# Performance work log

Hardware: AMD Instinct MI355X
Metric: run time of the kernel (lower is better)

## Reference

```python
import jax, jax.numpy as jnp
import numpy as np

N = 100_000
E = 1_600_000
D_IN, D_HID, D_OUT = 512, 256, 256


def setup_inputs() -> dict:
    key = jax.random.key(0)
    ks = jax.random.split(key, 10)
    x = jax.random.normal(ks[0], (N, D_IN), dtype=jnp.float32)
    edge_index = jax.random.randint(ks[1], (2, E), 0, N, dtype=jnp.int64)
    edge_weight = jax.random.uniform(ks[2], (E,), dtype=jnp.float32)
    # Glorot-ish init for the per-layer linear weights (PyG GCNConv: Linear w/o bias, bias added after aggregation)
    W1 = jax.random.normal(ks[3], (D_IN, D_HID), dtype=jnp.float32) * (1.0 / np.sqrt(D_IN))
    b1 = jnp.zeros((D_HID,), dtype=jnp.float32)
    W2 = jax.random.normal(ks[4], (D_HID, D_HID), dtype=jnp.float32) * (1.0 / np.sqrt(D_HID))
    b2 = jnp.zeros((D_HID,), dtype=jnp.float32)
    W3 = jax.random.normal(ks[5], (D_HID, D_OUT), dtype=jnp.float32) * (1.0 / np.sqrt(D_HID))
    b3 = jnp.zeros((D_OUT,), dtype=jnp.float32)
    return {"x": x, "edge_index": edge_index, "edge_weight": edge_weight,
            "W1": W1, "b1": b1, "W2": W2, "b2": b2, "W3": W3, "b3": b3}


def gcn_layer(h_in, W, b, row, col, ew, n):
    # PyG GCNConv with normalize=True, add_self_loops=True (fill value 1.0), aggr='add':
    # h = X W; deg[i] = sum of incoming edge weights (incl. self loop);
    # norm_e = deg^-1/2[row] * w_e * deg^-1/2[col]; out[col] += norm_e * h[row]; out += bias
    h = h_in @ W                                            # [n, d_out]
    deg = jnp.zeros((n,), h.dtype).at[col].add(ew) + 1.0    # +1 from self loop
    dinv = jnp.where(deg > 0, jax.lax.rsqrt(deg), 0.0)      # deg_inv_sqrt, inf -> 0
    norm = dinv[row] * ew * dinv[col]                       # [E]
    out = jnp.zeros_like(h).at[col].add(norm[:, None] * h[row])
    out = out + (dinv * dinv)[:, None] * h                  # self-loop contribution (norm_ii = dinv_i^2)
    return out + b


def reference(x, edge_index, edge_weight, W1, b1, W2, b2, W3, b3):
    row, col = edge_index[0], edge_index[1]
    n = x.shape[0]
    # dropout p=0.0 -> identity
    h = jax.nn.relu(gcn_layer(x, W1, b1, row, col, edge_weight, n))
    h = jax.nn.relu(gcn_layer(h, W2, b2, row, col, edge_weight, n))
    return gcn_layer(h, W3, b3, row, col, edge_weight, n)
```

## Files before the change

### kernel.cpp

```cpp
#include <hip/hip_runtime.h>
#include <hip/hip_bf16.h>


#define D 256
#define ELLW 48
#define BSH2 9
#define NB2MAX 256
#define DEPTH 24
#define GCAP 8960
#define FIXSCALE 1099511627776.0f
#define FIXINV   9.094947017729282e-13

typedef unsigned short ushort_t;
typedef unsigned long long u64;
typedef float f32x2 __attribute__((ext_vector_type(2)));
typedef float f32x4 __attribute__((ext_vector_type(4)));
typedef short bf16x8 __attribute__((ext_vector_type(8)));
typedef unsigned int u32x4 __attribute__((ext_vector_type(4)));

__device__ __forceinline__ float blo(unsigned u) { return __uint_as_float(u << 16); }
__device__ __forceinline__ float bhi(unsigned u) { return __uint_as_float(u & 0xFFFF0000u); }
__device__ __forceinline__ ushort_t f2b(float f) {
    unsigned u = __float_as_uint(f);
    return (ushort_t)((u + 0x7FFFu + ((u >> 16) & 1u)) >> 16);
}
__device__ __forceinline__ void gload_lds16(const ushort_t* g, ushort_t* l) {
    __builtin_amdgcn_global_load_lds((const __attribute__((address_space(1))) unsigned int*)g,
                                     (__attribute__((address_space(3))) unsigned int*)l, 16, 0, 0);
}

__global__ void zero_gfill(int* __restrict__ gfill, int nb) {
    if ((int)threadIdx.x < nb) gfill[threadIdx.x] = 0;
}

__global__ __launch_bounds__(1024) void bin_p1(const int* __restrict__ row,
                                               const int* __restrict__ col,
                                               const float* __restrict__ ew,
                                               int* __restrict__ gfill,
                                               u64* __restrict__ bins, int E, int nb) {
    __shared__ u64 lbuf[196][DEPTH];
    __shared__ int lcnt[196];
    __shared__ int sgp[196];
    const int t = threadIdx.x;
    const int wv = t >> 6, ln = t & 63;
    if (t < 196) lcnt[t] = 0;
    __syncthreads();
    int per = (E + gridDim.x - 1) / gridDim.x;
    int e0 = blockIdx.x * per;
    int e1 = e0 + per;
    if (e1 > E) e1 = E;
    for (int base = e0; base < e1; base += 1024) {
        int e = base + t;
        if (e < e1) {
            int c = __builtin_nontemporal_load(&col[e]);
            int r = __builtin_nontemporal_load(&row[e]);
            float w = __builtin_nontemporal_load(&ew[e]);
            int b = c >> BSH2;
            u64 rec = ((u64)__float_as_uint(w) << 32) | ((u64)(unsigned)r << 9) |
                      (unsigned)(c & ((1 << BSH2) - 1));
            int pos = atomicAdd(&lcnt[b], 1);
            if (pos < DEPTH) {
                lbuf[b][pos] = rec;
            } else {
                int gp = atomicAdd(&gfill[b], 1);
                if (gp < GCAP) bins[(size_t)b * GCAP + gp] = rec;
                atomicSub(&lcnt[b], 1);
            }
        }
        __syncthreads();
        if (t < nb) {
            int c = lcnt[t];
            int k8 = c & ~7;
            sgp[t] = (k8 > 0) ? atomicAdd(&gfill[t], k8) : 0;
        }
        __syncthreads();
        for (int b = wv; b < nb; b += 16) {
            int c = lcnt[b];
            int k8 = c & ~7;
            if (k8 > 0) {
                int gp = sgp[b];
                if (ln < k8) {
                    int idx = gp + ln;
                    if (idx < GCAP) bins[(size_t)b * GCAP + idx] = lbuf[b][ln];
                }
                int rem = c - k8;
                u64 mv = (ln < rem) ? lbuf[b][k8 + ln] : 0ull;
                if (ln < rem) lbuf[b][ln] = mv;
                if (ln == 0) lcnt[b] = rem;
            }
        }
        __syncthreads();
    }
    if (t < nb) {
        int c = lcnt[t];
        sgp[t] = (c > 0) ? atomicAdd(&gfill[t], c) : 0;
    }
    __syncthreads();
    for (int b = wv; b < nb; b += 16) {
        int c = lcnt[b];
        if (c > 0) {
            int gp = sgp[b];
            if (ln < c) {
                int idx = gp + ln;
                if (idx < GCAP) bins[(size_t)b * GCAP + idx] = lbuf[b][ln];
            }
        }
    }
}

__global__ __launch_bounds__(512) void bin_p2(const u64* __restrict__ bins,
                                              const int* __restrict__ gfill,
                                              int* __restrict__ cnt,
                                              float* __restrict__ dinv,
                                              u64* __restrict__ ell, int N) {
    __shared__ u64 sacc[1 << BSH2];
    const int b = blockIdx.x, t = threadIdx.x;
    const int base = b << BSH2;
    for (int i = t; i < (1 << BSH2); i += 512) sacc[i] = 0ull;
    __syncthreads();
    int fill = gfill[b];
    if (fill > GCAP) fill = GCAP;
    for (int i = t; i < fill; i += 512) {
        u64 rec = bins[(size_t)b * GCAP + i];
        int li = (int)(rec & ((1 << BSH2) - 1));
        unsigned r = (unsigned)((rec >> 9) & 0x1FFFFu);
        unsigned wb = (unsigned)(rec >> 32);
        u64 pack = (1ull << 48) | (u64)(__uint_as_float(wb) * FIXSCALE);
        int pos = (int)(atomicAdd(&sacc[li], pack) >> 48);
        if (pos < ELLW)
            ell[(size_t)(base + li) * ELLW + pos] = ((u64)wb << 32) | r;
    }
    __syncthreads();
    for (int i = t; i < (1 << BSH2); i += 512) {
        int node = base + i;
        if (node < N) {
            u64 p = sacc[i];
            int m = (int)(p >> 48);
            cnt[node] = (m > ELLW) ? ELLW : m;
            float sum = (float)((double)(p & 0xFFFFFFFFFFFFull) * FIXINV);
            dinv[node] = rsqrtf(sum + 1.0f);
        }
    }
}

__global__ __launch_bounds__(256) void cvtT_kernel(const float* __restrict__ W,
                                                   ushort_t* __restrict__ WT, int K, int C) {
    int i = blockIdx.x * 256 + threadIdx.x;
    if (i < K * C) {
        int c = i / K, k = i - c * K;
        WT[i] = f2b(W[(size_t)k * C + c]);
    }
}

template <int K, bool AF32>
__global__ __launch_bounds__(256) void gemm_mfma(const void* __restrict__ Ap,
                                                 const ushort_t* __restrict__ WT,
                                                 ushort_t* __restrict__ C, int nvalid) {
    __shared__ ushort_t As[128 * 64];
    __shared__ ushort_t Bs[256 * 64];
    const int tid = threadIdx.x;
    const int lane = tid & 63, wave = tid >> 6;
    const int wrow = wave >> 1, wcol = wave & 1;
    const int fr = lane & 15, fq = lane >> 4;
    const int r0 = blockIdx.x * 128;

    f32x4 acc[4][8] = {};

    for (int k0 = 0; k0 < K; k0 += 64) {
        if constexpr (AF32) {
            const float* Af = (const float*)Ap;
#pragma unroll
            for (int i = 0; i < 8; ++i) {
                int idx = i * 256 + tid;
                int rowt = idx >> 4;
                int c4 = idx & 15;
                int grow = r0 + rowt;
                if (grow >= nvalid) grow = nvalid - 1;
                f32x4 v = __builtin_nontemporal_load(
                    (const f32x4*)&Af[(size_t)grow * K + k0 + c4 * 4]);
                __hip_bfloat162 b01 = __float22bfloat162_rn(make_float2(v[0], v[1]));
                __hip_bfloat162 b23 = __float22bfloat162_rn(make_float2(v[2], v[3]));
                uint2 st = make_uint2(*(unsigned*)&b01, *(unsigned*)&b23);
                int slot = c4 >> 1, half = c4 & 1;
                int off = rowt * 64 + ((slot ^ (rowt & 7)) << 3) + (half << 2);
                *(uint2*)&As[off] = st;
            }
        } else {
            const ushort_t* Ab = (const ushort_t*)Ap;
#pragma unroll
            for (int q = 0; q < 4; ++q) {
                int qa = wave * 4 + q;
                int rowt = qa * 8 + (lane >> 3);
                int g = (lane & 7) ^ (lane >> 3);
                gload_lds16(&Ab[(size_t)(r0 + rowt) * K + k0 + g * 8], &As[qa * 512]);
            }
        }
#pragma unroll
        for (int q = 0; q < 8; ++q) {
            int qb = wave * 8 + q;
            int rowt = qb * 8 + (lane >> 3);
            int g = (lane & 7) ^ (lane >> 3);
            gload_lds16(&WT[(size_t)rowt * K + k0 + g * 8], &Bs[qb * 512]);
        }
        __syncthreads();

#pragma unroll
        for (int kk = 0; kk < 2; ++kk) {
            int g = (kk * 4 + fq) ^ (fr & 7);
            bf16x8 aF[4];
#pragma unroll
            for (int m = 0; m < 4; ++m) {
                int arow = wrow * 64 + m * 16 + fr;
                aF[m] = *(const bf16x8*)&As[arow * 64 + g * 8];
            }
#pragma unroll
            for (int n = 0; n < 8; ++n) {
                int bcol = wcol * 128 + n * 16 + fr;
                bf16x8 bF = *(const bf16x8*)&Bs[bcol * 64 + g * 8];
#pragma unroll
                for (int m = 0; m < 4; ++m)
                    acc[m][n] = __builtin_amdgcn_mfma_f32_16x16x32_bf16(
                        bF, aF[m], acc[m][n], 0, 0, 0);
            }
        }
        __syncthreads();
    }

#pragma unroll
    for (int m = 0; m < 4; ++m) {
        int gr = r0 + wrow * 64 + m * 16 + fr;
        if (gr < nvalid) {
#pragma unroll
            for (int n = 0; n < 8; ++n) {
                ushort4 h;
                h.x = f2b(acc[m][n][0]); h.y = f2b(acc[m][n][1]);
                h.z = f2b(acc[m][n][2]); h.w = f2b(acc[m][n][3]);
                *(ushort4*)&C[(size_t)gr * D + wcol * 128 + n * 16 + fq * 4] = h;
            }
        }
    }
}

template <bool NORM, bool RELU, bool OUTF32>
__global__ __launch_bounds__(256) void agg_kernel(const ushort_t* __restrict__ hb,
                                                  const float* __restrict__ dinv,
                                                  const float* __restrict__ bias,
                                                  const int* __restrict__ cnt,
                                                  u64* __restrict__ ell,
                                                  void* __restrict__ outp, int N) {
    int node = blockIdx.x * 4 + (threadIdx.x >> 6);
    if (node >= N) return;
    int lane = threadIdx.x & 63;
    int half = lane >> 5;
    int fl = lane & 31;
    float dn = dinv[node], d2 = dn * dn;

    u32x4 sv = *(const u32x4*)&hb[(size_t)node * 256 + fl * 8];
    float sc = half ? 0.f : d2;
    float a0 = sc * blo(sv.x), a1 = sc * bhi(sv.x);
    float a2 = sc * blo(sv.y), a3 = sc * bhi(sv.y);
    float a4 = sc * blo(sv.z), a5 = sc * bhi(sv.z);
    float a6 = sc * blo(sv.w), a7 = sc * bhi(sv.w);

    int m = cnt[node];
    int srcl = 0;
    float wl = 0.f;
    if (lane < m) {
        u64 r = ell[(size_t)node * ELLW + lane];
        srcl = (int)(unsigned)r;
        float w = __uint_as_float((unsigned)(r >> 32));
        if (NORM) {
            wl = dinv[srcl] * w * dn;
            ell[(size_t)node * ELLW + lane] =
                ((u64)__float_as_uint(wl) << 32) | (unsigned)srcl;
        } else {
            wl = w;
        }
    }
    int steps = (m + 1) >> 1;
#pragma unroll 8
    for (int j = 0; j < steps; ++j) {
        int idx2 = 2 * j + half;
        int src = __shfl(srcl, idx2);
        float w = __shfl(wl, idx2);
        u32x4 v = *(const u32x4*)&hb[(size_t)src * 256 + fl * 8];
        a0 = fmaf(w, blo(v.x), a0); a1 = fmaf(w, bhi(v.x), a1);
        a2 = fmaf(w, blo(v.y), a2); a3 = fmaf(w, bhi(v.y), a3);
        a4 = fmaf(w, blo(v.z), a4); a5 = fmaf(w, bhi(v.z), a5);
        a6 = fmaf(w, blo(v.w), a6); a7 = fmaf(w, bhi(v.w), a7);
    }
    a0 += __shfl_xor(a0, 32); a1 += __shfl_xor(a1, 32);
    a2 += __shfl_xor(a2, 32); a3 += __shfl_xor(a3, 32);
    a4 += __shfl_xor(a4, 32); a5 += __shfl_xor(a5, 32);
    a6 += __shfl_xor(a6, 32); a7 += __shfl_xor(a7, 32);
    float r0 = half ? a4 : a0;
    float r1 = half ? a5 : a1;
    float r2 = half ? a6 : a2;
    float r3 = half ? a7 : a3;
    f32x4 bb = *(const f32x4*)&bias[fl * 8 + half * 4];
    r0 += bb[0]; r1 += bb[1]; r2 += bb[2]; r3 += bb[3];
    if (RELU) {
        r0 = fmaxf(r0, 0.f); r1 = fmaxf(r1, 0.f);
        r2 = fmaxf(r2, 0.f); r3 = fmaxf(r3, 0.f);
    }
    if (OUTF32) {
        f32x4 o = {r0, r1, r2, r3};
        __builtin_nontemporal_store(
            o, (f32x4*)((float*)outp + (size_t)node * 256 + fl * 8 + half * 4));
    } else {
        u64 p = (u64)f2b(r0) | ((u64)f2b(r1) << 16) | ((u64)f2b(r2) << 32) | ((u64)f2b(r3) << 48);
        __builtin_nontemporal_store(
            p, (u64*)((ushort_t*)outp + (size_t)node * 256 + fl * 8 + half * 4));
    }
}

extern "C" void kernel_launch(void* const* d_in, const int* in_sizes, int n_in,
                              void* d_out, int out_size, void* d_ws, size_t ws_size,
                              hipStream_t stream) {
    const float* x  = (const float*)d_in[0];
    const int*   ei = (const int*)d_in[1];
    const float* ew = (const float*)d_in[2];
    const float* W1 = (const float*)d_in[3];
    const float* b1 = (const float*)d_in[4];
    const float* W2 = (const float*)d_in[5];
    const float* b2 = (const float*)d_in[6];
    const float* W3 = (const float*)d_in[7];
    const float* b3 = (const float*)d_in[8];
    const int N = in_sizes[0] / 512;
    const int E = in_sizes[2];
    const int* row = ei;
    const int* col = ei + E;
    float* out = (float*)d_out;

    const int MB = (N + 127) / 128;
    const size_t Npad = (size_t)MB * 128;
    const int NB2 = (N + (1 << BSH2) - 1) >> BSH2;

    char* ws = (char*)d_ws;
    size_t off = 0;
    auto alloc = [&](size_t bytes) -> void* {
        void* p = ws + off;
        off += (bytes + 255) / 256 * 256;
        return p;
    };
    ushort_t* hb  = (ushort_t*)alloc(Npad * D * sizeof(ushort_t));
    u64*      ell = (u64*)alloc((size_t)N * ELLW * sizeof(u64));
    ushort_t* WT1 = (ushort_t*)alloc((size_t)512 * D * sizeof(ushort_t));
    ushort_t* WT2 = (ushort_t*)alloc((size_t)256 * D * sizeof(ushort_t));
    ushort_t* WT3 = (ushort_t*)alloc((size_t)256 * D * sizeof(ushort_t));
    int*   cnt    = (int*)alloc((size_t)N * sizeof(int));
    float* dinv   = (float*)alloc((size_t)N * sizeof(float));
    int*   gfill  = (int*)alloc((size_t)NB2MAX * sizeof(int));
    u64*   bins   = (u64*)hb;
    ushort_t* ab  = (ushort_t*)d_out;

    int gA = (N + 3) / 4;
    zero_gfill<<<1, 256, 0, stream>>>(gfill, NB2);
    cvtT_kernel<<<(512 * D + 255) / 256, 256, 0, stream>>>(W1, WT1, 512, D);
    cvtT_kernel<<<(256 * D + 255) / 256, 256, 0, stream>>>(W2, WT2, 256, D);
    cvtT_kernel<<<(256 * D + 255) / 256, 256, 0, stream>>>(W3, WT3, 256, D);
    bin_p1<<<256, 1024, 0, stream>>>(row, col, ew, gfill, bins, E, NB2);
    bin_p2<<<NB2, 512, 0, stream>>>(bins, gfill, cnt, dinv, ell, N);

    gemm_mfma<512, true><<<MB, 256, 0, stream>>>(x, WT1, hb, N);
    agg_kernel<true, true, false><<<gA, 256, 0, stream>>>(hb, dinv, b1, cnt, ell, ab, N);
    gemm_mfma<256, false><<<MB, 256, 0, stream>>>(ab, WT2, hb, N);
    agg_kernel<false, true, false><<<gA, 256, 0, stream>>>(hb, dinv, b2, cnt, ell, ab, N);
    gemm_mfma<256, false><<<MB, 256, 0, stream>>>(ab, WT3, hb, N);
    agg_kernel<false, false, true><<<gA, 256, 0, stream>>>(hb, dinv, b3, cnt, ell, out, N);
}
```

Before: 635.4 us.

## Co-schedule edge binning with first GEMM in one heterogeneous kernel launch

Merges the three weight transpose/convert kernels and the gfill zeroing into a single prep kernel. Edge binning (now 512 blocks of 256 threads with a smaller local buffer depth) and the first-layer GEMM then run in one launch, with block IDs split between the two roles so the memory-bound binning overlaps the compute-bound GEMM. Because hb can no longer double as the bins buffer, bins get their own workspace allocation. The cost is extra workspace, plus possible imbalance or lower occupancy from the shared 48KB LDS footprint in the binning blocks.

```diff
diff --git a/kernel.cpp b/kernel.cpp
--- a/kernel.cpp
+++ b/kernel.cpp
@@ -6,7 +6,8 @@
 #define ELLW 48
 #define BSH2 9
 #define NB2MAX 256
-#define DEPTH 24
+#define DEPTH 16
+#define NBIN 512
 #define GCAP 8960
 #define FIXSCALE 1099511627776.0f
 #define FIXINV   9.094947017729282e-13
@@ -29,27 +30,47 @@
                                      (__attribute__((address_space(3))) unsigned int*)l, 16, 0, 0);
 }
 
-__global__ void zero_gfill(int* __restrict__ gfill, int nb) {
-    if ((int)threadIdx.x < nb) gfill[threadIdx.x] = 0;
-}
-
-__global__ __launch_bounds__(1024) void bin_p1(const int* __restrict__ row,
-                                               const int* __restrict__ col,
-                                               const float* __restrict__ ew,
-                                               int* __restrict__ gfill,
-                                               u64* __restrict__ bins, int E, int nb) {
-    __shared__ u64 lbuf[196][DEPTH];
-    __shared__ int lcnt[196];
-    __shared__ int sgp[196];
+__global__ __launch_bounds__(256) void prep_kernel(const float* __restrict__ W1,
+                                                   const float* __restrict__ W2,
+                                                   const float* __restrict__ W3,
+                                                   ushort_t* __restrict__ WT1,
+                                                   ushort_t* __restrict__ WT2,
+                                                   ushort_t* __restrict__ WT3,
+                                                   int* __restrict__ gfill, int nb) {
+    int i = blockIdx.x * 256 + threadIdx.x;
+    if (i < nb) gfill[i] = 0;
+    if (i < 131072) {
+        int c = i >> 9, k = i & 511;
+        WT1[i] = f2b(W1[k * 256 + c]);
+    } else if (i < 196608) {
+        int j = i - 131072;
+        int c = j >> 8, k = j & 255;
+        WT2[j] = f2b(W2[k * 256 + c]);
+    } else if (i < 262144) {
+        int j = i - 196608;
+        int c = j >> 8, k = j & 255;
+        WT3[j] = f2b(W3[k * 256 + c]);
+    }
+}
+
+__device__ __forceinline__ void bin_body(char* smem,
+                                         const int* __restrict__ row,
+                                         const int* __restrict__ col,
+                                         const float* __restrict__ ew,
+                                         int* __restrict__ gfill,
+                                         u64* __restrict__ bins, int E, int nb, int bid) {
+    u64 (*lbuf)[DEPTH] = (u64(*)[DEPTH])smem;
+    int* lcnt = (int*)(smem + 25088);
+    int* sgp  = (int*)(smem + 25088 + 784);
     const int t = threadIdx.x;
     const int wv = t >> 6, ln = t & 63;
     if (t < 196) lcnt[t] = 0;
     __syncthreads();
-    int per = (E + gridDim.x - 1) / gridDim.x;
-    int e0 = blockIdx.x * per;
+    int per = (E + NBIN - 1) / NBIN;
+    int e0 = bid * per;
     int e1 = e0 + per;
     if (e1 > E) e1 = E;
-    for (int base = e0; base < e1; base += 1024) {
+    for (int base = e0; base < e1; base += 256) {
         int e = base + t;
         if (e < e1) {
             int c = __builtin_nontemporal_load(&col[e]);
@@ -74,7 +95,7 @@
             sgp[t] = (k8 > 0) ? atomicAdd(&gfill[t], k8) : 0;
         }
         __syncthreads();
-        for (int b = wv; b < nb; b += 16) {
+        for (int b = wv; b < nb; b += 4) {
             int c = lcnt[b];
             int k8 = c & ~7;
             if (k8 > 0) {
@@ -96,7 +117,7 @@
         sgp[t] = (c > 0) ? atomicAdd(&gfill[t], c) : 0;
     }
     __syncthreads();
-    for (int b = wv; b < nb; b += 16) {
+    for (int b = wv; b < nb; b += 4) {
         int c = lcnt[b];
         if (c > 0) {
             int gp = sgp[b];
@@ -106,6 +127,121 @@
             }
         }
     }
+}
+
+template <int K, bool AF32>
+__device__ __forceinline__ void gemm_body(char* smem,
+                                          const void* __restrict__ Ap,
+                                          const ushort_t* __restrict__ WT,
+                                          ushort_t* __restrict__ C, int nvalid, int tile) {
+    ushort_t* As = (ushort_t*)smem;
+    ushort_t* Bs = (ushort_t*)(smem + 16384);
+    const int tid = threadIdx.x;
+    const int lane = tid & 63, wave = tid >> 6;
+    const int wrow = wave >> 1, wcol = wave & 1;
+    const int fr = lane & 15, fq = lane >> 4;
+    const int r0 = tile * 128;
+
+    f32x4 acc[4][8] = {};
+
+    for (int k0 = 0; k0 < K; k0 += 64) {
+        if constexpr (AF32) {
+            const float* Af = (const float*)Ap;
+#pragma unroll
+            for (int i = 0; i < 8; ++i) {
+                int idx = i * 256 + tid;
+                int rowt = idx >> 4;
+                int c4 = idx & 15;
+                int grow = r0 + rowt;
+                if (grow >= nvalid) grow = nvalid - 1;
+                f32x4 v = __builtin_nontemporal_load(
+                    (const f32x4*)&Af[(size_t)grow * K + k0 + c4 * 4]);
+                __hip_bfloat162 b01 = __float22bfloat162_rn(make_float2(v[0], v[1]));
+                __hip_bfloat162 b23 = __float22bfloat162_rn(make_float2(v[2], v[3]));
+                uint2 st = make_uint2(*(unsigned*)&b01, *(unsigned*)&b23);
+                int slot = c4 >> 1, half = c4 & 1;
+                int off = rowt * 64 + ((slot ^ (rowt & 7)) << 3) + (half << 2);
+                *(uint2*)&As[off] = st;
+            }
+        } else {
+            const ushort_t* Ab = (const ushort_t*)Ap;
+#pragma unroll
+            for (int q = 0; q < 4; ++q) {
+                int qa = wave * 4 + q;
+                int rowt = qa * 8 + (lane >> 3);
+                int g = (lane & 7) ^ (lane >> 3);
+                gload_lds16(&Ab[(size_t)(r0 + rowt) * K + k0 + g * 8], &As[qa * 512]);
+            }
+        }
+#pragma unroll
+        for (int q = 0; q < 8; ++q) {
+            int qb = wave * 8 + q;
+            int rowt = qb * 8 + (lane >> 3);
+            int g = (lane & 7) ^ (lane >> 3);
+            gload_lds16(&WT[(size_t)rowt * K + k0 + g * 8], &Bs[qb * 512]);
+        }
+        __syncthreads();
+
+#pragma unroll
+        for (int kk = 0; kk < 2; ++kk) {
+            int g = (kk * 4 + fq) ^ (fr & 7);
+            bf16x8 aF[4];
+#pragma unroll
+            for (int m = 0; m < 4; ++m) {
+                int arow = wrow * 64 + m * 16 + fr;
+                aF[m] = *(const bf16x8*)&As[arow * 64 + g * 8];
+            }
+#pragma unroll
+            for (int n = 0; n < 8; ++n) {
+                int bcol = wcol * 128 + n * 16 + fr;
+                bf16x8 bF = *(const bf16x8*)&Bs[bcol * 64 + g * 8];
+#pragma unroll
+                for (int m = 0; m < 4; ++m)
+                    acc[m][n] = __builtin_amdgcn_mfma_f32_16x16x32_bf16(
+                        bF, aF[m], acc[m][n], 0, 0, 0);
+            }
+        }
+        __syncthreads();
+    }
+
+#pragma unroll
+    for (int m = 0; m < 4; ++m) {
+        int gr = r0 + wrow * 64 + m * 16 + fr;
+        if (gr < nvalid) {
+#pragma unroll
+            for (int n = 0; n < 8; ++n) {
+                ushort4 h;
+                h.x = f2b(acc[m][n][0]); h.y = f2b(acc[m][n][1]);
+                h.z = f2b(acc[m][n][2]); h.w = f2b(acc[m][n][3]);
+                *(ushort4*)&C[(size_t)gr * D + wcol * 128 + n * 16 + fq * 4] = h;
+            }
+        }
+    }
+}
+
+__global__ __launch_bounds__(256) void gemm1_bin(const float* __restrict__ x,
+                                                 const ushort_t* __restrict__ WT1,
+                                                 ushort_t* __restrict__ hb, int N,
+                                                 const int* __restrict__ row,
+                                                 const int* __restrict__ col,
+                                                 const float* __restrict__ ew,
+                                                 int* __restrict__ gfill,
+                                                 u64* __restrict__ bins, int E, int nb) {
+    __shared__ __align__(16) char smem[49152];
+    int bid = blockIdx.x;
+    if (bid < NBIN) {
+        bin_body(smem, row, col, ew, gfill, bins, E, nb, bid);
+    } else {
+        gemm_body<512, true>(smem, x, WT1, hb, N, bid - NBIN);
+    }
+}
+
+template <int K, bool AF32>
+__global__ __launch_bounds__(256) void gemm_mfma(const void* __restrict__ Ap,
+                                                 const ushort_t* __restrict__ WT,
+                                                 ushort_t* __restrict__ C, int nvalid) {
+    __shared__ __align__(16) char smem[49152];
+    gemm_body<K, AF32>(smem, Ap, WT, C, nvalid, blockIdx.x);
 }
 
 __global__ __launch_bounds__(512) void bin_p2(const u64* __restrict__ bins,
@@ -143,104 +279,6 @@
     }
 }
 
-__global__ __launch_bounds__(256) void cvtT_kernel(const float* __restrict__ W,
-                                                   ushort_t* __restrict__ WT, int K, int C) {
-    int i = blockIdx.x * 256 + threadIdx.x;
-    if (i < K * C) {
-        int c = i / K, k = i - c * K;
-        WT[i] = f2b(W[(size_t)k * C + c]);
-    }
-}
-
-template <int K, bool AF32>
-__global__ __launch_bounds__(256) void gemm_mfma(const void* __restrict__ Ap,
-                                                 const ushort_t* __restrict__ WT,
-                                                 ushort_t* __restrict__ C, int nvalid) {
-    __shared__ ushort_t As[128 * 64];
-    __shared__ ushort_t Bs[256 * 64];
-    const int tid = threadIdx.x;
-    const int lane = tid & 63, wave = tid >> 6;
-    const int wrow = wave >> 1, wcol = wave & 1;
-    const int fr = lane & 15, fq = lane >> 4;
-    const int r0 = blockIdx.x * 128;
-
-    f32x4 acc[4][8] = {};
-
-    for (int k0 = 0; k0 < K; k0 += 64) {
-        if constexpr (AF32) {
-            const float* Af = (const float*)Ap;
-#pragma unroll
-            for (int i = 0; i < 8; ++i) {
-                int idx = i * 256 + tid;
-                int rowt = idx >> 4;
-                int c4 = idx & 15;
-                int grow = r0 + rowt;
-                if (grow >= nvalid) grow = nvalid - 1;
-                f32x4 v = __builtin_nontemporal_load(
-                    (const f32x4*)&Af[(size_t)grow * K + k0 + c4 * 4]);
-                __hip_bfloat162 b01 = __float22bfloat162_rn(make_float2(v[0], v[1]));
-                __hip_bfloat162 b23 = __float22bfloat162_rn(make_float2(v[2], v[3]));
-                uint2 st = make_uint2(*(unsigned*)&b01, *(unsigned*)&b23);
-                int slot = c4 >> 1, half = c4 & 1;
-                int off = rowt * 64 + ((slot ^ (rowt & 7)) << 3) + (half << 2);
-                *(uint2*)&As[off] = st;
-            }
-        } else {
-            const ushort_t* Ab = (const ushort_t*)Ap;
-#pragma unroll
-            for (int q = 0; q < 4; ++q) {
-                int qa = wave * 4 + q;
-                int rowt = qa * 8 + (lane >> 3);
-                int g = (lane & 7) ^ (lane >> 3);
-                gload_lds16(&Ab[(size_t)(r0 + rowt) * K + k0 + g * 8], &As[qa * 512]);
-            }
-        }
-#pragma unroll
-        for (int q = 0; q < 8; ++q) {
-            int qb = wave * 8 + q;
-            int rowt = qb * 8 + (lane >> 3);
-            int g = (lane & 7) ^ (lane >> 3);
-            gload_lds16(&WT[(size_t)rowt * K + k0 + g * 8], &Bs[qb * 512]);
-        }
-        __syncthreads();
-
-#pragma unroll
-        for (int kk = 0; kk < 2; ++kk) {
-            int g = (kk * 4 + fq) ^ (fr & 7);
-            bf16x8 aF[4];
-#pragma unroll
-            for (int m = 0; m < 4; ++m) {
-                int arow = wrow * 64 + m * 16 + fr;
-                aF[m] = *(const bf16x8*)&As[arow * 64 + g * 8];
-            }
-#pragma unroll
-            for (int n = 0; n < 8; ++n) {
-                int bcol = wcol * 128 + n * 16 + fr;
-                bf16x8 bF = *(const bf16x8*)&Bs[bcol * 64 + g * 8];
-#pragma unroll
-                for (int m = 0; m < 4; ++m)
-                    acc[m][n] = __builtin_amdgcn_mfma_f32_16x16x32_bf16(
-                        bF, aF[m], acc[m][n], 0, 0, 0);
-            }
-        }
-        __syncthreads();
-    }
-
-#pragma unroll
-    for (int m = 0; m < 4; ++m) {
-        int gr = r0 + wrow * 64 + m * 16 + fr;
-        if (gr < nvalid) {
-#pragma unroll
-            for (int n = 0; n < 8; ++n) {
-                ushort4 h;
-                h.x = f2b(acc[m][n][0]); h.y = f2b(acc[m][n][1]);
-                h.z = f2b(acc[m][n][2]); h.w = f2b(acc[m][n][3]);
-                *(ushort4*)&C[(size_t)gr * D + wcol * 128 + n * 16 + fq * 4] = h;
-            }
-        }
-    }
-}
-
 template <bool NORM, bool RELU, bool OUTF32>
 __global__ __launch_bounds__(256) void agg_kernel(const ushort_t* __restrict__ hb,
                                                   const float* __restrict__ dinv,
@@ -345,24 +383,20 @@
     };
     ushort_t* hb  = (ushort_t*)alloc(Npad * D * sizeof(ushort_t));
     u64*      ell = (u64*)alloc((size_t)N * ELLW * sizeof(u64));
+    u64*      bins = (u64*)alloc((size_t)NB2 * GCAP * sizeof(u64));
     ushort_t* WT1 = (ushort_t*)alloc((size_t)512 * D * sizeof(ushort_t));
     ushort_t* WT2 = (ushort_t*)alloc((size_t)256 * D * sizeof(ushort_t));
     ushort_t* WT3 = (ushort_t*)alloc((size_t)256 * D * sizeof(ushort_t));
     int*   cnt    = (int*)alloc((size_t)N * sizeof(int));
     float* dinv   = (float*)alloc((size_t)N * sizeof(float));
     int*   gfill  = (int*)alloc((size_t)NB2MAX * sizeof(int));
-    u64*   bins   = (u64*)hb;
     ushort_t* ab  = (ushort_t*)d_out;
 
     int gA = (N + 3) / 4;
-    zero_gfill<<<1, 256, 0, stream>>>(gfill, NB2);
-    cvtT_kernel<<<(512 * D + 255) / 256, 256, 0, stream>>>(W1, WT1, 512, D);
-    cvtT_kernel<<<(256 * D + 255) / 256, 256, 0, stream>>>(W2, WT2, 256, D);
-    cvtT_kernel<<<(256 * D + 255) / 256, 256, 0, stream>>>(W3, WT3, 256, D);
-    bin_p1<<<256, 1024, 0, stream>>>(row, col, ew, gfill, bins, E, NB2);
+    prep_kernel<<<1024, 256, 0, stream>>>(W1, W2, W3, WT1, WT2, WT3, gfill, NB2);
+    gemm1_bin<<<NBIN + MB, 256, 0, stream>>>(x, WT1, hb, N, row, col, ew, gfill, bins, E, NB2);
     bin_p2<<<NB2, 512, 0, stream>>>(bins, gfill, cnt, dinv, ell, N);
 
-    gemm_mfma<512, true><<<MB, 256, 0, stream>>>(x, WT1, hb, N);
     agg_kernel<true, true, false><<<gA, 256, 0, stream>>>(hb, dinv, b1, cnt, ell, ab, N);
     gemm_mfma<256, false><<<MB, 256, 0, stream>>>(ab, WT2, hb, N);
     agg_kernel<false, true, false><<<gA, 256, 0, stream>>>(hb, dinv, b2, cnt, ell, ab, N);
```

Result: slower. 694.0 us (+9.2%).
